# Performance work log

Measured on AMD Instinct MI355X. Metric: run time of the kernel, lower is better.

## Reference

```python
import jax, jax.numpy as jnp
import numpy as np

ANGSTROM_TO_BOHR = 1.8897261258369282
CUTOFF = 5.2  # angstrom
N_SPECIES = 4  # H, C, N, O

# GFN1-xTB-style per-element constants for (H, C, N, O)
_ALPHA = np.array([2.209700, 1.247655, 1.524329, 1.845886], dtype=np.float32)
_Y_EFF = np.array([1.116244, 4.428763, 5.498808, 5.171786], dtype=np.float32)


def _smooth_cutoff(d, rc, eps=1e-10):
    # torchani 'smooth' cutoff: exp(1 - 1/(1 - (d/rc)^2)) for d < rc, else 0
    x2 = (d / rc) ** 2
    e = 1.0 - 1.0 / jnp.maximum(1.0 - x2, eps)
    return jnp.where(d < rc, jnp.exp(e), jnp.zeros_like(d))


def setup_inputs() -> dict:
    key = jax.random.key(0)
    k1, k2, k3 = jax.random.split(key, 3)
    M, A, P = 2048, 64, 8388608
    element_idxs = jax.random.randint(k1, (M, A), 0, N_SPECIES, dtype=jnp.int64)
    neighbor_idxs = jax.random.randint(k2, (2, P), 0, M * A, dtype=jnp.int64)
    distances = jax.random.uniform(k3, (P,), dtype=jnp.float32, minval=0.5, maxval=6.0)
    # precomputed pairwise parameter tables (buffers in the torch module)
    y_ab = jnp.asarray(np.outer(_Y_EFF, _Y_EFF))                 # [4,4]
    sqrt_alpha_ab = jnp.asarray(np.sqrt(np.outer(_ALPHA, _ALPHA)))  # [4,4]
    k_rep = np.full((N_SPECIES, N_SPECIES), 1.5, dtype=np.float32)
    k_rep[0, 0] = 1.0  # H-H
    k_rep_ab = jnp.asarray(k_rep)
    return {
        "element_idxs": element_idxs,
        "neighbor_idxs": neighbor_idxs,
        "distances": distances,
        "y_ab": y_ab,
        "sqrt_alpha_ab": sqrt_alpha_ab,
        "k_rep_ab": k_rep_ab,
    }


def reference(element_idxs, neighbor_idxs, distances, y_ab, sqrt_alpha_ab, k_rep_ab):
    M, A = element_idxs.shape
    d = jnp.clip(distances, 1e-7) * ANGSTROM_TO_BOHR  # [P] bohr
    species12 = element_idxs.reshape(-1)[neighbor_idxs]  # [2, P]
    s0, s1 = species12[0], species12[1]
    y = y_ab[s0, s1]                    # [P] gather
    sa = sqrt_alpha_ab[s0, s1]          # [P]
    kr = k_rep_ab[s0, s1]               # [P]
    rep = (y / d) * jnp.exp(-sa * d ** kr)
    rep = rep * _smooth_cutoff(d, CUTOFF * ANGSTROM_TO_BOHR)
    mol_idx = neighbor_idxs[0] // A     # [P]
    energies = jax.ops.segment_sum(rep, mol_idx, num_segments=M)  # [M]
    return energies
```

## Files before the change

kernel.cpp:

```cpp
#include <hip/hip_runtime.h>


#define AB_D 1.8897261258369282
#define L2E  1.4426950408889634f

__global__ __launch_bounds__(256) void pack_zero_kernel(
    const int* __restrict__ elem, int natoms, int nwords,
    unsigned* __restrict__ packed, float* __restrict__ out, int M)
{
    int g = blockIdx.x * blockDim.x + threadIdx.x;
    if (g < M) out[g] = 0.0f;
    if (g < nwords) {
        int base = g * 16;
        unsigned w = 0u;
        if (base + 16 <= natoms) {
            const int4* p = (const int4*)(elem + base);
            #pragma unroll
            for (int q = 0; q < 4; ++q) {
                int4 v = p[q];
                w |= ((unsigned)v.x & 3u) << (2 * (4 * q + 0));
                w |= ((unsigned)v.y & 3u) << (2 * (4 * q + 1));
                w |= ((unsigned)v.z & 3u) << (2 * (4 * q + 2));
                w |= ((unsigned)v.w & 3u) << (2 * (4 * q + 3));
            }
        } else {
            for (int j = 0; j < 16; ++j) {
                int a = base + j;
                unsigned s = (a < natoms) ? ((unsigned)elem[a] & 3u) : 0u;
                w |= s << (2 * j);
            }
        }
        packed[g] = w;
    }
}

__device__ __forceinline__ float sel4(unsigned s, float a, float b, float c, float d)
{
    float lo = (s & 1u) ? b : a;
    float hi = (s & 1u) ? d : c;
    return (s & 2u) ? hi : lo;
}

__global__ __launch_bounds__(512, 6) void rep_main_kernel(
    const int* __restrict__ nbr, const float* __restrict__ dist,
    const unsigned* __restrict__ packed_g,
    const float* __restrict__ y_ab, const float* __restrict__ sa_ab,
    const float* __restrict__ kr_ab,
    long long P, int M, int nwords, int ashift, int A,
    float* __restrict__ out)
{
    extern __shared__ char smem[];
    float*    acc = (float*)smem;
    unsigned* pk  = (unsigned*)(smem + (size_t)M * 4);

    const int tid  = threadIdx.x;
    const int nthr = blockDim.x;

    for (int m = tid; m < M; m += nthr) acc[m] = 0.0f;
    for (int w = tid; w < nwords; w += nthr) pk[w] = packed_g[w];

    const float yv0 = sqrtf(y_ab[0]),  yv1 = sqrtf(y_ab[5]);
    const float yv2 = sqrtf(y_ab[10]), yv3 = sqrtf(y_ab[15]);
    const float sL2E = sqrtf(L2E);
    const float av0 = sqrtf(sa_ab[0])  * sL2E, av1 = sqrtf(sa_ab[5])  * sL2E;
    const float av2 = sqrtf(sa_ab[10]) * sL2E, av3 = sqrtf(sa_ab[15]) * sL2E;
    (void)kr_ab;
    __syncthreads();

    const float ABf   = (float)AB_D;
    const float RC    = (float)(5.2 * AB_D);
    const float RCINV = (float)(1.0 / (5.2 * AB_D));
    const int* nb0 = nbr;
    const int* nb1 = nbr + P;

    auto process_quad = [&](int4 i0, int4 i1, float4 dv) {
        unsigned a0[4] = {(unsigned)i0.x, (unsigned)i0.y, (unsigned)i0.z, (unsigned)i0.w};
        unsigned a1[4] = {(unsigned)i1.x, (unsigned)i1.y, (unsigned)i1.z, (unsigned)i1.w};
        float    dr[4] = {dv.x, dv.y, dv.z, dv.w};
        unsigned w0[4], w1[4];
        #pragma unroll
        for (int j = 0; j < 4; ++j) {
            w0[j] = pk[a0[j] >> 4];
            w1[j] = pk[a1[j] >> 4];
        }
        #pragma unroll
        for (int j = 0; j < 4; ++j) {
            unsigned s0 = (w0[j] >> ((a0[j] & 15u) * 2u)) & 3u;
            unsigned s1 = (w1[j] >> ((a1[j] & 15u) * 2u)) & 3u;
            float y  = sel4(s0, yv0, yv1, yv2, yv3) * sel4(s1, yv0, yv1, yv2, yv3);
            float sa = sel4(s0, av0, av1, av2, av3) * sel4(s1, av0, av1, av2, av3);

            float d    = dr[j] * ABf;
            float sq   = __builtin_amdgcn_sqrtf(d);
            float fac  = ((s0 | s1) == 0u) ? 1.0f : sq;
            float drep = d * fac;
            float x    = d * RCINV;
            float om   = fmaf(-x, x, 1.0f);
            float r    = __builtin_amdgcn_rcpf(om);
            float e    = fmaf(-L2E, r, L2E);
            float arg  = fmaf(-sa, drep, e);
            float ex   = __builtin_amdgcn_exp2f(arg);
            float rep  = y * __builtin_amdgcn_rcpf(d) * ex;
            rep = (d < RC) ? rep : 0.0f;

            unsigned mol = (ashift >= 0) ? (a0[j] >> ashift) : (a0[j] / (unsigned)A);
            atomicAdd(&acc[mol], rep);
        }
    };

    long long P4 = P >> 2;
    long long chunk = (P4 + gridDim.x - 1) / gridDim.x;
    long long start = (long long)blockIdx.x * chunk;
    long long end   = start + chunk; if (end > P4) end = P4;

    long long q = start + tid;
    bool valid = q < end;
    int4 A0, A1; float4 D0;
    if (valid) {
        A0 = ((const int4*)nb0)[q];
        A1 = ((const int4*)nb1)[q];
        D0 = ((const float4*)dist)[q];
    }
    while (valid) {
        long long q2 = q + nthr;
        bool v2 = q2 < end;
        int4 B0, B1; float4 E0;
        if (v2) {
            B0 = ((const int4*)nb0)[q2];
            B1 = ((const int4*)nb1)[q2];
            E0 = ((const float4*)dist)[q2];
        }
        process_quad(A0, A1, D0);
        valid = v2; q = q2;
        A0 = B0; A1 = B1; D0 = E0;
    }

    long long tail0 = P4 << 2;
    if (blockIdx.x == 0) {
        for (long long p = tail0 + tid; p < P; p += nthr) {
            unsigned ua0 = (unsigned)nb0[p], ua1 = (unsigned)nb1[p];
            unsigned s0 = (pk[ua0 >> 4] >> ((ua0 & 15u) * 2u)) & 3u;
            unsigned s1 = (pk[ua1 >> 4] >> ((ua1 & 15u) * 2u)) & 3u;
            float y  = sel4(s0, yv0, yv1, yv2, yv3) * sel4(s1, yv0, yv1, yv2, yv3);
            float sa = sel4(s0, av0, av1, av2, av3) * sel4(s1, av0, av1, av2, av3);
            float d    = dist[p] * ABf;
            float sq   = __builtin_amdgcn_sqrtf(d);
            float fac  = ((s0 | s1) == 0u) ? 1.0f : sq;
            float drep = d * fac;
            float x    = d * RCINV;
            float om   = fmaf(-x, x, 1.0f);
            float r    = __builtin_amdgcn_rcpf(om);
            float e    = fmaf(-L2E, r, L2E);
            float arg  = fmaf(-sa, drep, e);
            float rep  = y * __builtin_amdgcn_rcpf(d) * __builtin_amdgcn_exp2f(arg);
            rep = (d < RC) ? rep : 0.0f;
            unsigned mol = (ashift >= 0) ? (ua0 >> ashift) : (ua0 / (unsigned)A);
            atomicAdd(&acc[mol], rep);
        }
    }
    __syncthreads();

    for (int m = tid; m < M; m += nthr)
        atomicAdd(&out[m], acc[m]);
}

extern "C" void kernel_launch(void* const* d_in, const int* in_sizes, int n_in,
                              void* d_out, int out_size, void* d_ws, size_t ws_size,
                              hipStream_t stream)
{
    const int*   elem  = (const int*)d_in[0];
    const int*   nbr   = (const int*)d_in[1];
    const float* dist  = (const float*)d_in[2];
    const float* y_ab  = (const float*)d_in[3];
    const float* sa_ab = (const float*)d_in[4];
    const float* kr_ab = (const float*)d_in[5];
    float* out = (float*)d_out;

    const int natoms = in_sizes[0];
    const long long P = (long long)in_sizes[2];
    const int M = out_size;
    const int A = natoms / M;
    int ashift = -1;
    if (A > 0 && (A & (A - 1)) == 0) {
        int s = 0;
        while ((1 << s) < A) ++s;
        ashift = s;
    }
    const int nwords = (natoms + 15) / 16;

    if (ws_size < (size_t)nwords * 4) return;
    unsigned* packed = (unsigned*)d_ws;

    {
        int total = (nwords > M) ? nwords : M;
        int g = (total + 255) / 256;
        hipLaunchKernelGGL(pack_zero_kernel, dim3(g), dim3(256), 0, stream,
                           elem, natoms, nwords, packed, out, M);
    }

    {
        const int BLOCK = 512;
        const int nblk  = 768;
        size_t smem = (size_t)M * 4 + (size_t)nwords * 4;
        hipLaunchKernelGGL(rep_main_kernel, dim3(nblk), dim3(BLOCK), smem, stream,
                           nbr, dist, packed, y_ab, sa_ab, kr_ab,
                           P, M, nwords, ashift, A, out);
    }
}
```

Measured before the change: 160.3 us.

## Hash-swizzle chunk order, use 1024-thread blocks, and reduce partials in a separate kernel

Replaces per-block contiguous ranges with wavefront-granular 64-quad chunks, visited in a multiplicative-hash swizzled order and two chunks in flight per iteration. Blocks grow to 1024 threads across 512 blocks. When workspace allows, each block writes its molecule accumulator row to a partials buffer, and a second reduce kernel sums the rows instead of every block issuing global atomics. It also adds the missing distance clamp for correctness. The changes aim to cut global atomic contention and improve memory-level parallelism. In exchange they add an extra kernel launch and partials traffic, and the scattered chunk access may hurt DRAM locality.

```diff
diff --git a/kernel.cpp b/kernel.cpp
--- a/kernel.cpp
+++ b/kernel.cpp
@@ -41,13 +41,13 @@
     return (s & 2u) ? hi : lo;
 }
 
-__global__ __launch_bounds__(512, 6) void rep_main_kernel(
+__global__ __launch_bounds__(1024, 8) void rep_main_kernel(
     const int* __restrict__ nbr, const float* __restrict__ dist,
     const unsigned* __restrict__ packed_g,
     const float* __restrict__ y_ab, const float* __restrict__ sa_ab,
-    const float* __restrict__ kr_ab,
     long long P, int M, int nwords, int ashift, int A,
-    float* __restrict__ out)
+    unsigned cmask, int use_swz,
+    float* __restrict__ partials, float* __restrict__ out, int mode)
 {
     extern __shared__ char smem[];
     float*    acc = (float*)smem;
@@ -64,14 +64,34 @@
     const float sL2E = sqrtf(L2E);
     const float av0 = sqrtf(sa_ab[0])  * sL2E, av1 = sqrtf(sa_ab[5])  * sL2E;
     const float av2 = sqrtf(sa_ab[10]) * sL2E, av3 = sqrtf(sa_ab[15]) * sL2E;
-    (void)kr_ab;
     __syncthreads();
 
     const float ABf   = (float)AB_D;
+    const float DMIN  = (float)(1e-7 * AB_D);
     const float RC    = (float)(5.2 * AB_D);
     const float RCINV = (float)(1.0 / (5.2 * AB_D));
     const int* nb0 = nbr;
     const int* nb1 = nbr + P;
+
+    auto process_one = [&](unsigned ua0, unsigned ua1, float draw) {
+        unsigned s0 = (pk[ua0 >> 4] >> ((ua0 & 15u) * 2u)) & 3u;
+        unsigned s1 = (pk[ua1 >> 4] >> ((ua1 & 15u) * 2u)) & 3u;
+        float y  = sel4(s0, yv0, yv1, yv2, yv3) * sel4(s1, yv0, yv1, yv2, yv3);
+        float sa = sel4(s0, av0, av1, av2, av3) * sel4(s1, av0, av1, av2, av3);
+        float d    = fmaxf(draw * ABf, DMIN);
+        float sq   = __builtin_amdgcn_sqrtf(d);
+        float fac  = ((s0 | s1) == 0u) ? 1.0f : sq;
+        float drep = d * fac;
+        float x    = d * RCINV;
+        float om   = fmaf(-x, x, 1.0f);
+        float r    = __builtin_amdgcn_rcpf(om);
+        float e    = fmaf(-L2E, r, L2E);
+        float arg  = fmaf(-sa, drep, e);
+        float rep  = y * __builtin_amdgcn_rcpf(d) * __builtin_amdgcn_exp2f(arg);
+        rep = (d < RC) ? rep : 0.0f;
+        unsigned mol = (ashift >= 0) ? (ua0 >> ashift) : (ua0 / (unsigned)A);
+        atomicAdd(&acc[mol], rep);
+    };
 
     auto process_quad = [&](int4 i0, int4 i1, float4 dv) {
         unsigned a0[4] = {(unsigned)i0.x, (unsigned)i0.y, (unsigned)i0.z, (unsigned)i0.w};
@@ -89,61 +109,7 @@
             unsigned s1 = (w1[j] >> ((a1[j] & 15u) * 2u)) & 3u;
             float y  = sel4(s0, yv0, yv1, yv2, yv3) * sel4(s1, yv0, yv1, yv2, yv3);
             float sa = sel4(s0, av0, av1, av2, av3) * sel4(s1, av0, av1, av2, av3);
-
-            float d    = dr[j] * ABf;
-            float sq   = __builtin_amdgcn_sqrtf(d);
-            float fac  = ((s0 | s1) == 0u) ? 1.0f : sq;
-            float drep = d * fac;
-            float x    = d * RCINV;
-            float om   = fmaf(-x, x, 1.0f);
-            float r    = __builtin_amdgcn_rcpf(om);
-            float e    = fmaf(-L2E, r, L2E);
-            float arg  = fmaf(-sa, drep, e);
-            float ex   = __builtin_amdgcn_exp2f(arg);
-            float rep  = y * __builtin_amdgcn_rcpf(d) * ex;
-            rep = (d < RC) ? rep : 0.0f;
-
-            unsigned mol = (ashift >= 0) ? (a0[j] >> ashift) : (a0[j] / (unsigned)A);
-            atomicAdd(&acc[mol], rep);
-        }
-    };
-
-    long long P4 = P >> 2;
-    long long chunk = (P4 + gridDim.x - 1) / gridDim.x;
-    long long start = (long long)blockIdx.x * chunk;
-    long long end   = start + chunk; if (end > P4) end = P4;
-
-    long long q = start + tid;
-    bool valid = q < end;
-    int4 A0, A1; float4 D0;
-    if (valid) {
-        A0 = ((const int4*)nb0)[q];
-        A1 = ((const int4*)nb1)[q];
-        D0 = ((const float4*)dist)[q];
-    }
-    while (valid) {
-        long long q2 = q + nthr;
-        bool v2 = q2 < end;
-        int4 B0, B1; float4 E0;
-        if (v2) {
-            B0 = ((const int4*)nb0)[q2];
-            B1 = ((const int4*)nb1)[q2];
-            E0 = ((const float4*)dist)[q2];
-        }
-        process_quad(A0, A1, D0);
-        valid = v2; q = q2;
-        A0 = B0; A1 = B1; D0 = E0;
-    }
-
-    long long tail0 = P4 << 2;
-    if (blockIdx.x == 0) {
-        for (long long p = tail0 + tid; p < P; p += nthr) {
-            unsigned ua0 = (unsigned)nb0[p], ua1 = (unsigned)nb1[p];
-            unsigned s0 = (pk[ua0 >> 4] >> ((ua0 & 15u) * 2u)) & 3u;
-            unsigned s1 = (pk[ua1 >> 4] >> ((ua1 & 15u) * 2u)) & 3u;
-            float y  = sel4(s0, yv0, yv1, yv2, yv3) * sel4(s1, yv0, yv1, yv2, yv3);
-            float sa = sel4(s0, av0, av1, av2, av3) * sel4(s1, av0, av1, av2, av3);
-            float d    = dist[p] * ABf;
+            float d    = fmaxf(dr[j] * ABf, DMIN);
             float sq   = __builtin_amdgcn_sqrtf(d);
             float fac  = ((s0 | s1) == 0u) ? 1.0f : sq;
             float drep = d * fac;
@@ -154,14 +120,81 @@
             float arg  = fmaf(-sa, drep, e);
             float rep  = y * __builtin_amdgcn_rcpf(d) * __builtin_amdgcn_exp2f(arg);
             rep = (d < RC) ? rep : 0.0f;
-            unsigned mol = (ashift >= 0) ? (ua0 >> ashift) : (ua0 / (unsigned)A);
+            unsigned mol = (ashift >= 0) ? (a0[j] >> ashift) : (a0[j] / (unsigned)A);
             atomicAdd(&acc[mol], rep);
         }
+    };
+
+    const int  lane = tid & 63;
+    long long P4 = P >> 2;
+    long long C  = P4 >> 6;
+    long long W  = ((long long)gridDim.x * nthr) >> 6;
+    long long wg = (((long long)blockIdx.x * nthr + tid)) >> 6;
+
+    auto swz = [&](long long c) -> long long {
+        if (!use_swz) return c;
+        return (long long)(((unsigned)c * 2654435761u) & cmask);
+    };
+    auto load3 = [&](long long c, int4& i0, int4& i1, float4& dv) {
+        long long q = (c << 6) + lane;
+        i0 = ((const int4*)nb0)[q];
+        i1 = ((const int4*)nb1)[q];
+        dv = ((const float4*)dist)[q];
+    };
+
+    for (long long c = wg; c < C; c += 2 * W) {
+        long long cB = c + W;
+        bool hasB = (cB < C);
+        int4 A0, A1, B0, B1; float4 D0, D1;
+        load3(swz(c), A0, A1, D0);
+        if (hasB) load3(swz(cB), B0, B1, D1);
+        process_quad(A0, A1, D0);
+        if (hasB) process_quad(B0, B1, D1);
+    }
+
+    if (blockIdx.x == 0) {
+        for (long long q = (C << 6) + tid; q < P4; q += nthr) {
+            int4   i0 = ((const int4*)nb0)[q];
+            int4   i1 = ((const int4*)nb1)[q];
+            float4 dv = ((const float4*)dist)[q];
+            process_quad(i0, i1, dv);
+        }
+        for (long long p = (P4 << 2) + tid; p < P; p += nthr)
+            process_one((unsigned)nb0[p], (unsigned)nb1[p], dist[p]);
     }
     __syncthreads();
 
-    for (int m = tid; m < M; m += nthr)
-        atomicAdd(&out[m], acc[m]);
+    if (mode == 0) {
+        float* row = partials + (size_t)blockIdx.x * (size_t)M;
+        for (int m = tid; m < M; m += nthr) row[m] = acc[m];
+    } else {
+        for (int m = tid; m < M; m += nthr) {
+            float v = acc[m];
+            if (v != 0.0f) atomicAdd(&out[m], v);
+        }
+    }
+}
+
+__global__ __launch_bounds__(256) void reduce_kernel(
+    const float* __restrict__ partials, float* __restrict__ out,
+    int M, int nblk, int rows_per)
+{
+    int m = blockIdx.x * blockDim.x + threadIdx.x;
+    if (m >= M) return;
+    int r0 = blockIdx.y * rows_per;
+    int r1 = r0 + rows_per;
+    if (r1 > nblk) r1 = nblk;
+    if (r0 >= r1) return;
+    float s0 = 0.f, s1 = 0.f, s2 = 0.f, s3 = 0.f;
+    int r = r0;
+    for (; r + 3 < r1; r += 4) {
+        s0 += partials[(size_t)(r + 0) * M + m];
+        s1 += partials[(size_t)(r + 1) * M + m];
+        s2 += partials[(size_t)(r + 2) * M + m];
+        s3 += partials[(size_t)(r + 3) * M + m];
+    }
+    for (; r < r1; ++r) s0 += partials[(size_t)r * M + m];
+    atomicAdd(&out[m], (s0 + s1) + (s2 + s3));
 }
 
 extern "C" void kernel_launch(void* const* d_in, const int* in_sizes, int n_in,
@@ -173,7 +206,6 @@
     const float* dist  = (const float*)d_in[2];
     const float* y_ab  = (const float*)d_in[3];
     const float* sa_ab = (const float*)d_in[4];
-    const float* kr_ab = (const float*)d_in[5];
     float* out = (float*)d_out;
 
     const int natoms = in_sizes[0];
@@ -188,8 +220,29 @@
     }
     const int nwords = (natoms + 15) / 16;
 
-    if (ws_size < (size_t)nwords * 4) return;
+    long long P4 = P >> 2;
+    long long C  = P4 >> 6;
+    int use_swz = (C > 1 && (C & (C - 1)) == 0) ? 1 : 0;
+    unsigned cmask = use_swz ? (unsigned)(C - 1) : 0u;
+
+    size_t packed_bytes = ((size_t)nwords * 4 + 255) & ~(size_t)255;
+    if (ws_size < packed_bytes) return;
     unsigned* packed = (unsigned*)d_ws;
+
+    const int BLOCK = 1024;
+    int nblk = 512;
+    float* partials = nullptr;
+    int mode = 1;
+    {
+        size_t avail = ws_size - packed_bytes;
+        size_t rowb = (size_t)M * 4;
+        long long maxrows = (long long)(avail / rowb);
+        if (maxrows >= 64) {
+            nblk = (int)(maxrows < 512 ? maxrows : 512);
+            partials = (float*)((char*)d_ws + packed_bytes);
+            mode = 0;
+        }
+    }
 
     {
         int total = (nwords > M) ? nwords : M;
@@ -199,11 +252,18 @@
     }
 
     {
-        const int BLOCK = 512;
-        const int nblk  = 768;
         size_t smem = (size_t)M * 4 + (size_t)nwords * 4;
         hipLaunchKernelGGL(rep_main_kernel, dim3(nblk), dim3(BLOCK), smem, stream,
-                           nbr, dist, packed, y_ab, sa_ab, kr_ab,
-                           P, M, nwords, ashift, A, out);
-    }
-}
+                           nbr, dist, packed, y_ab, sa_ab,
+                           P, M, nwords, ashift, A, cmask, use_swz,
+                           partials, out, mode);
+    }
+
+    if (mode == 0) {
+        const int SPLIT = 32;
+        int rows_per = (nblk + SPLIT - 1) / SPLIT;
+        dim3 grid((M + 255) / 256, SPLIT);
+        hipLaunchKernelGGL(reduce_kernel, grid, dim3(256), 0, stream,
+                           partials, out, M, nblk, rows_per);
+    }
+}
```

Result: no change. 158.6 us (-1.0%).
